# Performance work log

Measured on AMD Instinct MI355X. Metric: run time of the kernel, lower is better.

## Reference

```python
import jax, jax.numpy as jnp
import numpy as np

EMB = 1024
HEADS = 16
HEAD_DIM = EMB // HEADS
FF = 4 * EMB


def _gelu_tanh(x):
    c = jnp.sqrt(jnp.asarray(2.0 / jnp.pi, x.dtype))
    return 0.5 * x * (1.0 + jnp.tanh(c * (x + 0.044715 * x ** 3)))


def _layernorm(x, scale, shift, eps=1e-5):
    mean = jnp.mean(x, axis=-1, keepdims=True)
    var = jnp.mean((x - mean) ** 2, axis=-1, keepdims=True)
    return scale * (x - mean) / jnp.sqrt(var + eps) + shift


def setup_inputs() -> dict:
    key = jax.random.key(0)
    ks = jax.random.split(key, 8)
    s = 0.02
    return {
        "x": jax.random.normal(ks[0], (2, 2048, EMB), jnp.float32),
        "w_q": jax.random.normal(ks[1], (EMB, EMB), jnp.float32) * s,
        "w_k": jax.random.normal(ks[2], (EMB, EMB), jnp.float32) * s,
        "w_v": jax.random.normal(ks[3], (EMB, EMB), jnp.float32) * s,
        "w_o": jax.random.normal(ks[4], (EMB, EMB), jnp.float32) * s,
        "b_o": jnp.zeros((EMB,), jnp.float32),
        "ln1_scale": jnp.ones((EMB,), jnp.float32),
        "ln1_shift": jnp.zeros((EMB,), jnp.float32),
        "ln2_scale": jnp.ones((EMB,), jnp.float32),
        "ln2_shift": jnp.zeros((EMB,), jnp.float32),
        "w_ff1": jax.random.normal(ks[5], (EMB, FF), jnp.float32) * s,
        "b_ff1": jnp.zeros((FF,), jnp.float32),
        "w_ff2": jax.random.normal(ks[6], (FF, EMB), jnp.float32) * s,
        "b_ff2": jnp.zeros((EMB,), jnp.float32),
    }


def _attention(x, w_q, w_k, w_v, w_o, b_o):
    b, n, _ = x.shape
    q = (x @ w_q).reshape(b, n, HEADS, HEAD_DIM).transpose(0, 2, 1, 3)  # bhnd
    k = (x @ w_k).reshape(b, n, HEADS, HEAD_DIM).transpose(0, 2, 1, 3)
    v = (x @ w_v).reshape(b, n, HEADS, HEAD_DIM).transpose(0, 2, 1, 3)
    scores = jnp.einsum("bhqd,bhkd->bhqk", q, k)
    causal = jnp.triu(jnp.ones((n, n), bool), k=1)
    scores = jnp.where(causal, -jnp.inf, scores)
    # original scales AFTER masking (-inf stays -inf)
    attn = jax.nn.softmax(scores / jnp.sqrt(jnp.asarray(HEAD_DIM, x.dtype)), axis=-1)
    ctx = jnp.einsum("bhqk,bhkd->bhqd", attn, v)
    ctx = ctx.transpose(0, 2, 1, 3).reshape(b, n, EMB)
    return ctx @ w_o + b_o


def reference(x, w_q, w_k, w_v, w_o, b_o, ln1_scale, ln1_shift,
              ln2_scale, ln2_shift, w_ff1, b_ff1, w_ff2, b_ff2):
    h = _layernorm(x, ln1_scale, ln1_shift)
    h = _attention(h, w_q, w_k, w_v, w_o, b_o)
    x = x + h  # dropout is identity at drop_rate=0 / eval
    h = _layernorm(x, ln2_scale, ln2_shift)
    h = _gelu_tanh(h @ w_ff1 + b_ff1) @ w_ff2 + b_ff2
    return x + h
```

## Files before the change

kernel.cpp:

```cpp
#include <hip/hip_runtime.h>
#include <math.h>

#define EMB 1024
#define HEADS 16
#define HD 64
#define FF_DIM 4096
#define SEQ 2048
#define BATCH 2
#define NTOK (BATCH * SEQ)

typedef __bf16 bf16x8 __attribute__((ext_vector_type(8)));
typedef float f32x4 __attribute__((ext_vector_type(4)));

__device__ __forceinline__ unsigned short f2bf(float f) {
    union { float f; unsigned int u; } v; v.f = f;
    unsigned int r = v.u + 0x7fff + ((v.u >> 16) & 1);
    return (unsigned short)(r >> 16);
}

__device__ __forceinline__ float gelu_f(float x) {
    const float A = 1.5957691216057308f;
    const float B = 0.07135481282989427f;
    float zz = x * (A + B * x * x);
    return x * __builtin_amdgcn_rcpf(1.f + __expf(-zz));
}

#define GLOAD_LDS16(g, l)                                                      \
    __builtin_amdgcn_global_load_lds(                                          \
        (const __attribute__((address_space(1))) void*)(g),                    \
        (__attribute__((address_space(3))) void*)(l), 16, 0, 0)

__global__ __launch_bounds__(256) void ln_kernel(const float* __restrict__ x,
                                                 const float* __restrict__ scale,
                                                 const float* __restrict__ shift,
                                                 unsigned short* __restrict__ out) {
    int row = blockIdx.x;
    const float* xr = x + (size_t)row * EMB;
    unsigned short* yr = out + (size_t)row * EMB;
    int t = threadIdx.x;

    float v[4];
    float s = 0.f, s2 = 0.f;
#pragma unroll
    for (int i = 0; i < 4; i++) {
        v[i] = xr[t + i * 256];
        s += v[i];
        s2 += v[i] * v[i];
    }
    for (int o = 32; o > 0; o >>= 1) {
        s += __shfl_down(s, o, 64);
        s2 += __shfl_down(s2, o, 64);
    }
    __shared__ float red[4], red2[4];
    int wave = t >> 6;
    if ((t & 63) == 0) { red[wave] = s; red2[wave] = s2; }
    __syncthreads();
    if (t == 0) {
        float a = 0.f, b = 0.f;
#pragma unroll
        for (int i = 0; i < 4; i++) { a += red[i]; b += red2[i]; }
        red[0] = a; red2[0] = b;
    }
    __syncthreads();
    float mean = red[0] * (1.f / EMB);
    float var = red2[0] * (1.f / EMB) - mean * mean;
    float rstd = rsqrtf(var + 1e-5f);
#pragma unroll
    for (int i = 0; i < 4; i++) {
        int c = t + i * 256;
        yr[c] = f2bf(scale[c] * (v[i] - mean) * rstd + shift[c]);
    }
}

__global__ __launch_bounds__(256) void prep_kernel(
    const float* __restrict__ w0, const float* __restrict__ w1,
    const float* __restrict__ w2, const float* __restrict__ w3,
    const float* __restrict__ w4, const float* __restrict__ w5,
    unsigned short* __restrict__ o0, unsigned short* __restrict__ o1,
    unsigned short* __restrict__ o2, unsigned short* __restrict__ o3,
    unsigned short* __restrict__ o4, unsigned short* __restrict__ o5,
    const float* __restrict__ x, const float* __restrict__ ln1s,
    const float* __restrict__ ln1b, unsigned short* __restrict__ lnO) {
    __shared__ float tile[64][65];
    __shared__ float red[4], red2[4];
    int id = blockIdx.x;
    int t = threadIdx.x;

    if (id >= 3072) {
        int row = id - 3072;
        const float* xr = x + (size_t)row * EMB;
        unsigned short* yr = lnO + (size_t)row * EMB;
        float v[4];
        float s = 0.f, s2 = 0.f;
#pragma unroll
        for (int i = 0; i < 4; i++) {
            v[i] = xr[t + i * 256];
            s += v[i];
            s2 += v[i] * v[i];
        }
        for (int o = 32; o > 0; o >>= 1) {
            s += __shfl_down(s, o, 64);
            s2 += __shfl_down(s2, o, 64);
        }
        int wave = t >> 6;
        if ((t & 63) == 0) { red[wave] = s; red2[wave] = s2; }
        __syncthreads();
        if (t == 0) {
            float a = 0.f, b = 0.f;
#pragma unroll
            for (int i = 0; i < 4; i++) { a += red[i]; b += red2[i]; }
            red[0] = a; red2[0] = b;
        }
        __syncthreads();
        float mean = red[0] * (1.f / EMB);
        float var = red2[0] * (1.f / EMB) - mean * mean;
        float rstd = rsqrtf(var + 1e-5f);
#pragma unroll
        for (int i = 0; i < 4; i++) {
            int c = t + i * 256;
            yr[c] = f2bf(ln1s[c] * (v[i] - mean) * rstd + ln1b[c]);
        }
        return;
    }

    const float* src; unsigned short* dst; int K, N, lid;
    if (id < 256)       { src = w0; dst = o0; K = 1024; N = 1024; lid = id; }
    else if (id < 512)  { src = w1; dst = o1; K = 1024; N = 1024; lid = id - 256; }
    else if (id < 768)  { src = w2; dst = o2; K = 1024; N = 1024; lid = id - 512; }
    else if (id < 1024) { src = w3; dst = o3; K = 1024; N = 1024; lid = id - 768; }
    else if (id < 2048) { src = w4; dst = o4; K = 1024; N = 4096; lid = id - 1024; }
    else                { src = w5; dst = o5; K = 4096; N = 1024; lid = id - 2048; }
    int tn = N >> 6;
    int k0 = (lid / tn) << 6, n0 = (lid % tn) << 6;
    int rr = t >> 6, cc = t & 63;
#pragma unroll
    for (int i = 0; i < 16; i++) {
        int r = i * 4 + rr;
        tile[r][cc] = src[(size_t)(k0 + r) * N + n0 + cc];
    }
    __syncthreads();
#pragma unroll
    for (int i = 0; i < 16; i++) {
        int r = i * 4 + rr;
        dst[(size_t)(n0 + r) * K + k0 + cc] = f2bf(tile[cc][r]);
    }
}


__global__ __launch_bounds__(256) void ff1_gemm(
    const unsigned short* __restrict__ A,
    const unsigned short* __restrict__ Bt,
    unsigned short* __restrict__ C,
    const float* __restrict__ bias,
    int M, int N, int K) {
    __shared__ unsigned short As[2][128 * 64];
    __shared__ unsigned short Bs[2][128 * 64];

    const int t = threadIdx.x;
    const int w = t >> 6, lane = t & 63;
    const int m0 = blockIdx.x * 128, n0 = blockIdx.y * 128;

    const int srow = lane >> 3;
    const int sc = (lane & 7) ^ srow;
    const unsigned short* gA[4];
    const unsigned short* gB[4];
#pragma unroll
    for (int i = 0; i < 4; i++) {
        gA[i] = A + (size_t)(m0 + i * 32 + w * 8 + srow) * K + sc * 8;
        gB[i] = Bt + (size_t)(n0 + i * 32 + w * 8 + srow) * K + sc * 8;
    }

    const int mrow = (w >> 1) * 64, ncol = (w & 1) * 64;
    int ph[2];
#pragma unroll
    for (int s = 0; s < 2; s++) ph[s] = ((s * 4 + (lane >> 4)) ^ (lane & 7)) * 8;
    int abase[4], bbase[4];
#pragma unroll
    for (int i = 0; i < 4; i++) {
        abase[i] = (mrow + i * 16 + (lane & 15)) * 64;
        bbase[i] = (ncol + i * 16 + (lane & 15)) * 64;
    }

    f32x4 acc[4][4];
#pragma unroll
    for (int i = 0; i < 4; i++)
#pragma unroll
        for (int j = 0; j < 4; j++) acc[i][j] = (f32x4){0.f, 0.f, 0.f, 0.f};

#define STG1(b)                                                                \
    do {                                                                       \
        _Pragma("unroll") for (int i_ = 0; i_ < 4; i_++) {                     \
            GLOAD_LDS16(gA[i_], &As[b][(i_ * 32 + w * 8) * 64]);               \
            GLOAD_LDS16(gB[i_], &Bs[b][(i_ * 32 + w * 8) * 64]);               \
            gA[i_] += 64; gB[i_] += 64;                                        \
        }                                                                      \
    } while (0)

    STG1(0);
    const int nk = K >> 6;
    for (int it = 0; it < nk; it++) {
        const int buf = it & 1;
        __syncthreads();
        if (it + 1 < nk) STG1(buf ^ 1);
#pragma unroll
        for (int s = 0; s < 2; s++) {
            bf16x8 af[4], bfr[4];
#pragma unroll
            for (int i = 0; i < 4; i++) {
                af[i] = *reinterpret_cast<const bf16x8*>(&As[buf][abase[i] + ph[s]]);
                bfr[i] = *reinterpret_cast<const bf16x8*>(&Bs[buf][bbase[i] + ph[s]]);
            }
#pragma unroll
            for (int i = 0; i < 4; i++)
#pragma unroll
                for (int j = 0; j < 4; j++)
                    acc[i][j] = __builtin_amdgcn_mfma_f32_16x16x32_bf16(
                        af[i], bfr[j], acc[i][j], 0, 0, 0);
        }
    }
#undef STG1

    const int ccol = lane & 15;
    const int crow = (lane >> 4) << 2;
#pragma unroll
    for (int i = 0; i < 4; i++) {
#pragma unroll
        for (int j = 0; j < 4; j++) {
            int col = n0 + ncol + j * 16 + ccol;
            float badd = bias[col];
#pragma unroll
            for (int r = 0; r < 4; r++) {
                int row = m0 + mrow + i * 16 + crow + r;
                C[(size_t)row * N + col] = f2bf(gelu_f(acc[i][j][r] + badd));
            }
        }
    }
}

template <int EPI>
__global__ __launch_bounds__(256) void mfma_gemm_s64(
    const unsigned short* __restrict__ A,
    const unsigned short* __restrict__ Bt,
    float* __restrict__ C,
    const float* __restrict__ bias,
    const float* __restrict__ resid,
    int M, int N, int K) {
    __shared__ unsigned short As[2][64 * 64];
    __shared__ unsigned short Bs[2][64 * 64];

    const int t = threadIdx.x;
    const int w = t >> 6, lane = t & 63;
    const int m0 = blockIdx.x * 64, n0 = blockIdx.y * 64;

    const int srow = lane >> 3;
    const int sc = (lane & 7) ^ srow;
    const unsigned short* gA[2];
    const unsigned short* gB[2];
#pragma unroll
    for (int i = 0; i < 2; i++) {
        gA[i] = A + (size_t)(m0 + i * 32 + w * 8 + srow) * K + sc * 8;
        gB[i] = Bt + (size_t)(n0 + i * 32 + w * 8 + srow) * K + sc * 8;
    }

    int ph[2];
#pragma unroll
    for (int s = 0; s < 2; s++) ph[s] = ((s * 4 + (lane >> 4)) ^ (lane & 7)) * 8;
    const int mrow = (w >> 1) * 32, ncol = (w & 1) * 32;
    int abase[2], bbase[2];
#pragma unroll
    for (int i = 0; i < 2; i++) {
        abase[i] = (mrow + i * 16 + (lane & 15)) * 64;
        bbase[i] = (ncol + i * 16 + (lane & 15)) * 64;
    }

    f32x4 acc[2][2];
#pragma unroll
    for (int i = 0; i < 2; i++)
#pragma unroll
        for (int j = 0; j < 2; j++) acc[i][j] = (f32x4){0.f, 0.f, 0.f, 0.f};

#define STGS(b)                                                                \
    do {                                                                       \
        _Pragma("unroll") for (int i_ = 0; i_ < 2; i_++) {                     \
            GLOAD_LDS16(gA[i_], &As[b][(i_ * 32 + w * 8) * 64]);               \
            GLOAD_LDS16(gB[i_], &Bs[b][(i_ * 32 + w * 8) * 64]);               \
            gA[i_] += 64; gB[i_] += 64;                                        \
        }                                                                      \
    } while (0)

    STGS(0);
    const int nk = K >> 6;
    for (int it = 0; it < nk; it++) {
        const int buf = it & 1;
        __syncthreads();
        if (it + 1 < nk) STGS(buf ^ 1);
#pragma unroll
        for (int s = 0; s < 2; s++) {
            bf16x8 af[2], bfr[2];
#pragma unroll
            for (int i = 0; i < 2; i++) {
                af[i] = *reinterpret_cast<const bf16x8*>(&As[buf][abase[i] + ph[s]]);
                bfr[i] = *reinterpret_cast<const bf16x8*>(&Bs[buf][bbase[i] + ph[s]]);
            }
#pragma unroll
            for (int i = 0; i < 2; i++)
#pragma unroll
                for (int j = 0; j < 2; j++)
                    acc[i][j] = __builtin_amdgcn_mfma_f32_16x16x32_bf16(
                        af[i], bfr[j], acc[i][j], 0, 0, 0);
        }
    }
#undef STGS

    const int ccol = lane & 15;
    const int crow = (lane >> 4) << 2;
#pragma unroll
    for (int i = 0; i < 2; i++) {
#pragma unroll
        for (int j = 0; j < 2; j++) {
            int col = n0 + ncol + j * 16 + ccol;
            float badd = bias[col];
#pragma unroll
            for (int r = 0; r < 4; r++) {
                int row = m0 + mrow + i * 16 + crow + r;
                size_t idx = (size_t)row * N + col;
                if constexpr (EPI == 1) {
                    C[idx] = acc[i][j][r] + badd + resid[idx];
                } else {
                    C[idx] = C[idx] + acc[i][j][r] + badd;
                }
            }
        }
    }
}

__global__ __launch_bounds__(256) void qkv_gemm(
    const unsigned short* __restrict__ lnO,
    const unsigned short* __restrict__ wqkT,
    const unsigned short* __restrict__ wvT,
    unsigned short* __restrict__ q,
    unsigned short* __restrict__ kb,
    unsigned short* __restrict__ vT) {
    __shared__ unsigned short As[2][128 * 64];
    __shared__ unsigned short Bs[2][128 * 64];

    const int t = threadIdx.x;
    const int w = t >> 6, lane = t & 63;
    const int bid = blockIdx.x;
    const bool qk = bid < 512;

    const unsigned short *A, *Bt;
    int m0, n0, N;
    if (qk) {
        A = lnO; Bt = wqkT;
        m0 = (bid & 31) * 128; n0 = (bid >> 5) * 128; N = 2048;
    } else {
        int lb = bid - 512;
        A = wvT; Bt = lnO;
        m0 = (lb & 7) * 128; n0 = (lb >> 3) * 128; N = 4096;
    }
    const int K = 1024;

    const int srow = lane >> 3;
    const int sc = (lane & 7) ^ srow;
    const unsigned short* gA[4];
    const unsigned short* gB[4];
#pragma unroll
    for (int i = 0; i < 4; i++) {
        gA[i] = A + (size_t)(m0 + i * 32 + w * 8 + srow) * K + sc * 8;
        gB[i] = Bt + (size_t)(n0 + i * 32 + w * 8 + srow) * K + sc * 8;
    }

    const int mrow = (w >> 1) * 64, ncol = (w & 1) * 64;
    int ph[2];
#pragma unroll
    for (int s = 0; s < 2; s++) ph[s] = ((s * 4 + (lane >> 4)) ^ (lane & 7)) * 8;
    int abase[4], bbase[4];
#pragma unroll
    for (int i = 0; i < 4; i++) {
        abase[i] = (mrow + i * 16 + (lane & 15)) * 64;
        bbase[i] = (ncol + i * 16 + (lane & 15)) * 64;
    }

    f32x4 acc[4][4];
#pragma unroll
    for (int i = 0; i < 4; i++)
#pragma unroll
        for (int j = 0; j < 4; j++) acc[i][j] = (f32x4){0.f, 0.f, 0.f, 0.f};

#define STGQ(b)                                                                \
    do {                                                                       \
        _Pragma("unroll") for (int i_ = 0; i_ < 4; i_++) {                     \
            GLOAD_LDS16(gA[i_], &As[b][(i_ * 32 + w * 8) * 64]);               \
            GLOAD_LDS16(gB[i_], &Bs[b][(i_ * 32 + w * 8) * 64]);               \
            gA[i_] += 64; gB[i_] += 64;                                        \
        }                                                                      \
    } while (0)

    STGQ(0);
    const int nk = K >> 6;
    for (int it = 0; it < nk; it++) {
        const int buf = it & 1;
        __syncthreads();
        if (it + 1 < nk) STGQ(buf ^ 1);
#pragma unroll
        for (int s = 0; s < 2; s++) {
            bf16x8 af[4], bfr[4];
#pragma unroll
            for (int i = 0; i < 4; i++) {
                af[i] = *reinterpret_cast<const bf16x8*>(&As[buf][abase[i] + ph[s]]);
                bfr[i] = *reinterpret_cast<const bf16x8*>(&Bs[buf][bbase[i] + ph[s]]);
            }
#pragma unroll
            for (int i = 0; i < 4; i++)
#pragma unroll
                for (int j = 0; j < 4; j++)
                    acc[i][j] = __builtin_amdgcn_mfma_f32_16x16x32_bf16(
                        af[i], bfr[j], acc[i][j], 0, 0, 0);
        }
    }
#undef STGQ

    const int ccol = lane & 15;
    const int crow = (lane >> 4) << 2;
    unsigned short* dst;
    int nbase;
    if (qk) {
        dst = (n0 < 1024) ? q : kb;
        nbase = n0 & 1023;
    } else {
        dst = vT;
        nbase = n0;
    }
    const int ldc = qk ? 1024 : 4096;
#pragma unroll
    for (int i = 0; i < 4; i++) {
#pragma unroll
        for (int j = 0; j < 4; j++) {
            int col = nbase + ncol + j * 16 + ccol;
#pragma unroll
            for (int r = 0; r < 4; r++) {
                int row = m0 + mrow + i * 16 + crow + r;
                dst[(size_t)row * ldc + col] = f2bf(acc[i][j][r]);
            }
        }
    }
}

__global__ __launch_bounds__(256) void attn_mfma(
    const unsigned short* __restrict__ Q,
    const unsigned short* __restrict__ K,
    const unsigned short* __restrict__ Vt,
    unsigned short* __restrict__ O) {
    __shared__ unsigned short Ks[2][64 * 64];
    __shared__ unsigned short Vs[2][64 * 64];
    __shared__ unsigned short Ps[4][16 * 64];

    const int t = threadIdx.x;
    const int w = t >> 6, lane = t & 63;
    const int l15 = lane & 15, l4 = lane >> 4;
    const int bh = blockIdx.x;
    const int b = bh >> 4, h = bh & 15;
    const int pair = blockIdx.y;

    const int sr = (w << 3) + (lane >> 3);
    const int sc = lane & 7;
    const int c = sc ^ (sr & 7);
    const unsigned short* kbase = K + ((size_t)(b * SEQ)) * EMB + h * HD;
    const unsigned short* vbase = Vt + ((size_t)(h * HD)) * (size_t)NTOK + (size_t)b * SEQ;
    unsigned short* Pw = &Ps[w][0];

#define STAGE(k0s, buf)                                                        \
    do {                                                                       \
        GLOAD_LDS16(kbase + (size_t)((k0s) + sr) * EMB + c * 8,                \
                    &Ks[buf][(w << 3) * 64]);                                  \
        GLOAD_LDS16(kbase + (size_t)((k0s) + sr + 32) * EMB + c * 8,           \
                    &Ks[buf][((w << 3) + 32) * 64]);                           \
        GLOAD_LDS16(vbase + (size_t)sr * NTOK + (k0s) + c * 8,                 \
                    &Vs[buf][(w << 3) * 64]);                                  \
        GLOAD_LDS16(vbase + (size_t)(sr + 32) * NTOK + (k0s) + c * 8,          \
                    &Vs[buf][((w << 3) + 32) * 64]);                           \
    } while (0)

    const float C1 = 0.125f * 1.4426950408889634f;
    const float C2 = 3.0f * 1.4426950408889634f;

#pragma unroll
    for (int phase = 0; phase < 2; phase++) {
        const int qt = phase ? pair : (31 - pair);
        const int q0 = qt * 64;

        const unsigned short* qg =
            Q + ((size_t)(b * SEQ + q0 + w * 16 + l15)) * EMB + h * HD + l4 * 8;
        bf16x8 qf0 = *(const bf16x8*)qg;
        bf16x8 qf1 = *(const bf16x8*)(qg + 32);
        const int qrow_c = q0 + w * 16 + l4 * 4;

        float lsum[4] = {0.f, 0.f, 0.f, 0.f};
        f32x4 Oacc[4];
#pragma unroll
        for (int j = 0; j < 4; j++) Oacc[j] = (f32x4){0.f, 0.f, 0.f, 0.f};

        const int ntiles = qt + 1;
        __syncthreads();
        STAGE(0, 0);
        for (int tile = 0; tile < ntiles; tile++) {
            const int k0 = tile * 64;
            const int buf = tile & 1;
            __syncthreads();
            if (tile + 1 < ntiles) STAGE(k0 + 64, buf ^ 1);

            f32x4 S[4];
#pragma unroll
            for (int j = 0; j < 4; j++) S[j] = (f32x4){0.f, 0.f, 0.f, 0.f};
#pragma unroll
            for (int s = 0; s < 2; s++) {
                bf16x8 qf = s ? qf1 : qf0;
#pragma unroll
                for (int j = 0; j < 4; j++) {
                    int rk = 16 * j + l15;
                    int phys = (s * 4 + l4) ^ (rk & 7);
                    bf16x8 kf = *(const bf16x8*)&Ks[buf][rk * 64 + phys * 8];
                    S[j] = __builtin_amdgcn_mfma_f32_16x16x32_bf16(qf, kf, S[j], 0, 0, 0);
                }
            }

            if (tile == ntiles - 1) {
#pragma unroll
                for (int j = 0; j < 4; j++)
#pragma unroll
                    for (int r = 0; r < 4; r++) {
                        float e = exp2f(S[j][r] * C1 - C2);
                        if (k0 + 16 * j + l15 > qrow_c + r) e = 0.f;
                        S[j][r] = e;
                        lsum[r] += e;
                    }
            } else {
#pragma unroll
                for (int j = 0; j < 4; j++)
#pragma unroll
                    for (int r = 0; r < 4; r++) {
                        float e = exp2f(S[j][r] * C1 - C2);
                        S[j][r] = e;
                        lsum[r] += e;
                    }
            }

#pragma unroll
            for (int r = 0; r < 4; r++) {
                int row = l4 * 4 + r;
#pragma unroll
                for (int j = 0; j < 4; j++) {
                    int col = 16 * j + l15;
                    int phys = (col >> 3) ^ (row & 7);
                    Pw[row * 64 + phys * 8 + (col & 7)] = f2bf(S[j][r]);
                }
            }

#pragma unroll
            for (int s = 0; s < 2; s++) {
                int pphys = (s * 4 + l4) ^ (l15 & 7);
                bf16x8 pf = *(const bf16x8*)&Pw[l15 * 64 + pphys * 8];
#pragma unroll
                for (int j = 0; j < 4; j++) {
                    int rv = 16 * j + l15;
                    int vphys = (s * 4 + l4) ^ (rv & 7);
                    bf16x8 vf = *(const bf16x8*)&Vs[buf][rv * 64 + vphys * 8];
                    Oacc[j] = __builtin_amdgcn_mfma_f32_16x16x32_bf16(pf, vf, Oacc[j], 0, 0, 0);
                }
            }
        }

#pragma unroll
        for (int r = 0; r < 4; r++) {
            float l = lsum[r];
#pragma unroll
            for (int off = 1; off < 16; off <<= 1)
                l += __shfl_xor(l, off, 64);
            float inv = 1.f / l;
            size_t rowb = (size_t)(b * SEQ + qrow_c + r) * EMB + h * HD;
#pragma unroll
            for (int j = 0; j < 4; j++)
                O[rowb + 16 * j + l15] = f2bf(Oacc[j][r] * inv);
        }
    }
#undef STAGE
}

extern "C" void kernel_launch(void* const* d_in, const int* in_sizes, int n_in,
                              void* d_out, int out_size, void* d_ws, size_t ws_size,
                              hipStream_t stream) {
    const float* x     = (const float*)d_in[0];
    const float* w_q   = (const float*)d_in[1];
    const float* w_k   = (const float*)d_in[2];
    const float* w_v   = (const float*)d_in[3];
    const float* w_o   = (const float*)d_in[4];
    const float* b_o   = (const float*)d_in[5];
    const float* ln1s  = (const float*)d_in[6];
    const float* ln1b  = (const float*)d_in[7];
    const float* ln2s  = (const float*)d_in[8];
    const float* ln2b  = (const float*)d_in[9];
    const float* w_ff1 = (const float*)d_in[10];
    const float* b_ff1 = (const float*)d_in[11];
    const float* w_ff2 = (const float*)d_in[12];
    const float* b_ff2 = (const float*)d_in[13];
    float* out = (float*)d_out;

    char* p = (char*)d_ws;
    unsigned short* lnO  = (unsigned short*)p; p += (size_t)NTOK * EMB * 2;
    unsigned short* q    = (unsigned short*)p; p += (size_t)NTOK * EMB * 2;
    unsigned short* kbuf = (unsigned short*)p; p += (size_t)NTOK * EMB * 2;
    unsigned short* vT   = (unsigned short*)p; p += (size_t)NTOK * EMB * 2;
    unsigned short* ctx  = (unsigned short*)p; p += (size_t)NTOK * EMB * 2;
    unsigned short* ff1a = (unsigned short*)p; p += (size_t)NTOK * FF_DIM * 2;
    unsigned short* wqkT = (unsigned short*)p; p += (size_t)2 * EMB * EMB * 2;
    unsigned short* wvT  = (unsigned short*)p; p += (size_t)EMB * EMB * 2;
    unsigned short* woT  = (unsigned short*)p; p += (size_t)EMB * EMB * 2;
    unsigned short* wf1T = (unsigned short*)p; p += (size_t)FF_DIM * EMB * 2;
    unsigned short* wf2T = (unsigned short*)p; p += (size_t)EMB * FF_DIM * 2;

    dim3 blk(256);
    dim3 gS64(NTOK / 64, EMB / 64);
    dim3 gFF1(NTOK / 128, FF_DIM / 128);
    dim3 gAttn(BATCH * HEADS, 16);

    prep_kernel<<<3072 + NTOK, blk, 0, stream>>>(
        w_q, w_k, w_v, w_o, w_ff1, w_ff2,
        wqkT, wqkT + (size_t)EMB * EMB, wvT, woT, wf1T, wf2T,
        x, ln1s, ln1b, lnO);
    qkv_gemm<<<768, blk, 0, stream>>>(lnO, wqkT, wvT, q, kbuf, vT);
    attn_mfma<<<gAttn, blk, 0, stream>>>(q, kbuf, vT, ctx);
    mfma_gemm_s64<1><<<gS64, blk, 0, stream>>>(ctx, woT, out, b_o, x, NTOK, EMB, EMB);
    ln_kernel<<<NTOK, blk, 0, stream>>>(out, ln2s, ln2b, ctx);
    ff1_gemm<<<gFF1, blk, 0, stream>>>(ctx, wf1T, ff1a, b_ff1, NTOK, FF_DIM, EMB);
    mfma_gemm_s64<3><<<gS64, blk, 0, stream>>>(ff1a, wf2T, out, b_ff2, nullptr, NTOK, EMB, FF_DIM);
}
```

Before: 331.0 us.

## Add 128x128 FF2 GEMM kernel and transpose attention MFMA layout for packed stores

Replaces the 64x64-tiled FF2 GEMM (K=4096) with a dedicated 128x128-tile kernel using double-buffered global-to-LDS loads. This raises operand reuse per block and reduces the block count to 256. In attention, the MFMA operands are swapped so each lane holds four consecutive key columns. That lets P be written to LDS and O to global memory with packed bf16 conversions and 8-byte stores, and it replaces the per-row 16-lane shuffle reductions with two shuffles. The risk is that 256 blocks may underfill the GPU's compute units, and the larger accumulator tile raises register pressure.

```diff
diff --git a/kernel.cpp b/kernel.cpp
--- a/kernel.cpp
+++ b/kernel.cpp
@@ -16,6 +16,12 @@
     union { float f; unsigned int u; } v; v.f = f;
     unsigned int r = v.u + 0x7fff + ((v.u >> 16) & 1);
     return (unsigned short)(r >> 16);
+}
+
+__device__ __forceinline__ unsigned int cvt_pk_bf16(float a, float b) {
+    unsigned int r;
+    asm("v_cvt_pk_bf16_f32 %0, %1, %2" : "=v"(r) : "v"(a), "v"(b));
+    return r;
 }
 
 __device__ __forceinline__ float gelu_f(float x) {
@@ -237,6 +243,98 @@
     }
 }
 
+__global__ __launch_bounds__(256) void ff2_gemm(
+    const unsigned short* __restrict__ A,
+    const unsigned short* __restrict__ Bt,
+    float* __restrict__ C,
+    const float* __restrict__ bias,
+    int M, int N, int K) {
+    __shared__ unsigned short As[2][128 * 64];
+    __shared__ unsigned short Bs[2][128 * 64];
+
+    const int t = threadIdx.x;
+    const int w = t >> 6, lane = t & 63;
+    const int id = blockIdx.x;
+    const int m0 = (id >> 3) * 128, n0 = (id & 7) * 128;
+
+    const int srow = lane >> 3;
+    const int sc = (lane & 7) ^ srow;
+    const unsigned short* gA[4];
+    const unsigned short* gB[4];
+#pragma unroll
+    for (int i = 0; i < 4; i++) {
+        gA[i] = A + (size_t)(m0 + i * 32 + w * 8 + srow) * K + sc * 8;
+        gB[i] = Bt + (size_t)(n0 + i * 32 + w * 8 + srow) * K + sc * 8;
+    }
+
+    const int mrow = (w >> 1) * 64, ncol = (w & 1) * 64;
+    int ph[2];
+#pragma unroll
+    for (int s = 0; s < 2; s++) ph[s] = ((s * 4 + (lane >> 4)) ^ (lane & 7)) * 8;
+    int abase[4], bbase[4];
+#pragma unroll
+    for (int i = 0; i < 4; i++) {
+        abase[i] = (mrow + i * 16 + (lane & 15)) * 64;
+        bbase[i] = (ncol + i * 16 + (lane & 15)) * 64;
+    }
+
+    f32x4 acc[4][4];
+#pragma unroll
+    for (int i = 0; i < 4; i++)
+#pragma unroll
+        for (int j = 0; j < 4; j++) acc[i][j] = (f32x4){0.f, 0.f, 0.f, 0.f};
+
+#define STG2(b)                                                                \
+    do {                                                                       \
+        _Pragma("unroll") for (int i_ = 0; i_ < 4; i_++) {                     \
+            GLOAD_LDS16(gA[i_], &As[b][(i_ * 32 + w * 8) * 64]);               \
+            GLOAD_LDS16(gB[i_], &Bs[b][(i_ * 32 + w * 8) * 64]);               \
+            gA[i_] += 64; gB[i_] += 64;                                        \
+        }                                                                      \
+    } while (0)
+
+    STG2(0);
+    const int nk = K >> 6;
+    for (int it = 0; it < nk; it++) {
+        const int buf = it & 1;
+        __syncthreads();
+        if (it + 1 < nk) STG2(buf ^ 1);
+#pragma unroll
+        for (int s = 0; s < 2; s++) {
+            bf16x8 af[4], bfr[4];
+#pragma unroll
+            for (int i = 0; i < 4; i++) {
+                af[i] = *reinterpret_cast<const bf16x8*>(&As[buf][abase[i] + ph[s]]);
+                bfr[i] = *reinterpret_cast<const bf16x8*>(&Bs[buf][bbase[i] + ph[s]]);
+            }
+#pragma unroll
+            for (int i = 0; i < 4; i++)
+#pragma unroll
+                for (int j = 0; j < 4; j++)
+                    acc[i][j] = __builtin_amdgcn_mfma_f32_16x16x32_bf16(
+                        af[i], bfr[j], acc[i][j], 0, 0, 0);
+        }
+    }
+#undef STG2
+
+    const int ccol = lane & 15;
+    const int crow = (lane >> 4) << 2;
+#pragma unroll
+    for (int i = 0; i < 4; i++) {
+#pragma unroll
+        for (int j = 0; j < 4; j++) {
+            int col = n0 + ncol + j * 16 + ccol;
+            float badd = bias[col];
+#pragma unroll
+            for (int r = 0; r < 4; r++) {
+                int row = m0 + mrow + i * 16 + crow + r;
+                size_t idx = (size_t)row * N + col;
+                C[idx] = C[idx] + acc[i][j][r] + badd;
+            }
+        }
+    }
+}
+
 template <int EPI>
 __global__ __launch_bounds__(256) void mfma_gemm_s64(
     const unsigned short* __restrict__ A,
@@ -494,9 +592,9 @@
             Q + ((size_t)(b * SEQ + q0 + w * 16 + l15)) * EMB + h * HD + l4 * 8;
         bf16x8 qf0 = *(const bf16x8*)qg;
         bf16x8 qf1 = *(const bf16x8*)(qg + 32);
-        const int qrow_c = q0 + w * 16 + l4 * 4;
-
-        float lsum[4] = {0.f, 0.f, 0.f, 0.f};
+        const int qrow = q0 + w * 16 + l15;
+
+        float ls[4] = {0.f, 0.f, 0.f, 0.f};
         f32x4 Oacc[4];
 #pragma unroll
         for (int j = 0; j < 4; j++) Oacc[j] = (f32x4){0.f, 0.f, 0.f, 0.f};
@@ -521,7 +619,7 @@
                     int rk = 16 * j + l15;
                     int phys = (s * 4 + l4) ^ (rk & 7);
                     bf16x8 kf = *(const bf16x8*)&Ks[buf][rk * 64 + phys * 8];
-                    S[j] = __builtin_amdgcn_mfma_f32_16x16x32_bf16(qf, kf, S[j], 0, 0, 0);
+                    S[j] = __builtin_amdgcn_mfma_f32_16x16x32_bf16(kf, qf, S[j], 0, 0, 0);
                 }
             }
 
@@ -531,57 +629,52 @@
 #pragma unroll
                     for (int r = 0; r < 4; r++) {
                         float e = exp2f(S[j][r] * C1 - C2);
-                        if (k0 + 16 * j + l15 > qrow_c + r) e = 0.f;
+                        if (k0 + 16 * j + 4 * l4 + r > qrow) e = 0.f;
                         S[j][r] = e;
-                        lsum[r] += e;
                     }
             } else {
 #pragma unroll
                 for (int j = 0; j < 4; j++)
 #pragma unroll
-                    for (int r = 0; r < 4; r++) {
-                        float e = exp2f(S[j][r] * C1 - C2);
-                        S[j][r] = e;
-                        lsum[r] += e;
-                    }
-            }
-
-#pragma unroll
-            for (int r = 0; r < 4; r++) {
-                int row = l4 * 4 + r;
-#pragma unroll
-                for (int j = 0; j < 4; j++) {
-                    int col = 16 * j + l15;
-                    int phys = (col >> 3) ^ (row & 7);
-                    Pw[row * 64 + phys * 8 + (col & 7)] = f2bf(S[j][r]);
-                }
+                    for (int r = 0; r < 4; r++)
+                        S[j][r] = exp2f(S[j][r] * C1 - C2);
+            }
+
+#pragma unroll
+            for (int j = 0; j < 4; j++) {
+                ls[j] += S[j][0] + S[j][1] + S[j][2] + S[j][3];
+                unsigned int lo = cvt_pk_bf16(S[j][0], S[j][1]);
+                unsigned int hi = cvt_pk_bf16(S[j][2], S[j][3]);
+                int chunk = (2 * j + (l4 >> 1)) ^ (l15 & 7);
+                uint2 val; val.x = lo; val.y = hi;
+                *reinterpret_cast<uint2*>(&Pw[l15 * 64 + chunk * 8 + (l4 & 1) * 4]) = val;
             }
 
 #pragma unroll
             for (int s = 0; s < 2; s++) {
-                int pphys = (s * 4 + l4) ^ (l15 & 7);
-                bf16x8 pf = *(const bf16x8*)&Pw[l15 * 64 + pphys * 8];
+                int pch = (4 * s + l4) ^ (l15 & 7);
+                bf16x8 pf = *(const bf16x8*)&Pw[l15 * 64 + pch * 8];
 #pragma unroll
                 for (int j = 0; j < 4; j++) {
                     int rv = 16 * j + l15;
-                    int vphys = (s * 4 + l4) ^ (rv & 7);
-                    bf16x8 vf = *(const bf16x8*)&Vs[buf][rv * 64 + vphys * 8];
-                    Oacc[j] = __builtin_amdgcn_mfma_f32_16x16x32_bf16(pf, vf, Oacc[j], 0, 0, 0);
+                    int vph = (s * 4 + l4) ^ (rv & 7);
+                    bf16x8 vf = *(const bf16x8*)&Vs[buf][rv * 64 + vph * 8];
+                    Oacc[j] = __builtin_amdgcn_mfma_f32_16x16x32_bf16(vf, pf, Oacc[j], 0, 0, 0);
                 }
             }
         }
 
-#pragma unroll
-        for (int r = 0; r < 4; r++) {
-            float l = lsum[r];
-#pragma unroll
-            for (int off = 1; off < 16; off <<= 1)
-                l += __shfl_xor(l, off, 64);
-            float inv = 1.f / l;
-            size_t rowb = (size_t)(b * SEQ + qrow_c + r) * EMB + h * HD;
-#pragma unroll
-            for (int j = 0; j < 4; j++)
-                O[rowb + 16 * j + l15] = f2bf(Oacc[j][r] * inv);
+        float l = ls[0] + ls[1] + ls[2] + ls[3];
+        l += __shfl_xor(l, 16, 64);
+        l += __shfl_xor(l, 32, 64);
+        float inv = 1.f / l;
+        size_t rowb = (size_t)(b * SEQ + qrow) * EMB + h * HD;
+#pragma unroll
+        for (int j = 0; j < 4; j++) {
+            unsigned int lo = cvt_pk_bf16(Oacc[j][0] * inv, Oacc[j][1] * inv);
+            unsigned int hi = cvt_pk_bf16(Oacc[j][2] * inv, Oacc[j][3] * inv);
+            uint2 val; val.x = lo; val.y = hi;
+            *reinterpret_cast<uint2*>(&O[rowb + 16 * j + 4 * l4]) = val;
         }
     }
 #undef STAGE
@@ -633,5 +726,5 @@
     mfma_gemm_s64<1><<<gS64, blk, 0, stream>>>(ctx, woT, out, b_o, x, NTOK, EMB, EMB);
     ln_kernel<<<NTOK, blk, 0, stream>>>(out, ln2s, ln2b, ctx);
     ff1_gemm<<<gFF1, blk, 0, stream>>>(ctx, wf1T, ff1a, b_ff1, NTOK, FF_DIM, EMB);
-    mfma_gemm_s64<3><<<gS64, blk, 0, stream>>>(ff1a, wf2T, out, b_ff2, nullptr, NTOK, EMB, FF_DIM);
-}
+    ff2_gemm<<<256, blk, 0, stream>>>(ff1a, wf2T, out, b_ff2, NTOK, EMB, FF_DIM);
+}
```

Result: slower. 354.1 us (+7.0%).

## Transpose attention MFMA operands for packed P writes and vectorize layernorm

Applied to the files above, without the earlier changes.

Swaps the A/B operands of both attention MFMAs so each lane holds four consecutive key columns of one query row. P can then be written to LDS as packed bf16 pairs (v_cvt_pk_bf16) in 8-byte stores instead of scalar stores, and the output is written with vector stores. The row-sum reduction needs only two shuffles, and s_setprio is raised around the MFMA blocks. The layernorm kernels switch to float4 loads and ushort4 stores. This targets LDS store count and softmax overhead in the attention inner loop. It relies on the inline-asm conversion rounding the same way as the software f2bf.

```diff
diff --git a/kernel.cpp b/kernel.cpp
--- a/kernel.cpp
+++ b/kernel.cpp
@@ -18,6 +18,12 @@
     return (unsigned short)(r >> 16);
 }
 
+__device__ __forceinline__ unsigned int cvt_pk_bf16(float a, float b) {
+    unsigned int r;
+    asm("v_cvt_pk_bf16_f32 %0, %1, %2" : "=v"(r) : "v"(a), "v"(b));
+    return r;
+}
+
 __device__ __forceinline__ float gelu_f(float x) {
     const float A = 1.5957691216057308f;
     const float B = 0.07135481282989427f;
@@ -35,18 +41,12 @@
                                                  const float* __restrict__ shift,
                                                  unsigned short* __restrict__ out) {
     int row = blockIdx.x;
-    const float* xr = x + (size_t)row * EMB;
-    unsigned short* yr = out + (size_t)row * EMB;
+    const float4* xr = (const float4*)(x + (size_t)row * EMB);
     int t = threadIdx.x;
 
-    float v[4];
-    float s = 0.f, s2 = 0.f;
-#pragma unroll
-    for (int i = 0; i < 4; i++) {
-        v[i] = xr[t + i * 256];
-        s += v[i];
-        s2 += v[i] * v[i];
-    }
+    float4 v = xr[t];
+    float s = v.x + v.y + v.z + v.w;
+    float s2 = v.x * v.x + v.y * v.y + v.z * v.z + v.w * v.w;
     for (int o = 32; o > 0; o >>= 1) {
         s += __shfl_down(s, o, 64);
         s2 += __shfl_down(s2, o, 64);
@@ -65,11 +65,15 @@
     float mean = red[0] * (1.f / EMB);
     float var = red2[0] * (1.f / EMB) - mean * mean;
     float rstd = rsqrtf(var + 1e-5f);
-#pragma unroll
-    for (int i = 0; i < 4; i++) {
-        int c = t + i * 256;
-        yr[c] = f2bf(scale[c] * (v[i] - mean) * rstd + shift[c]);
-    }
+
+    float4 sc = ((const float4*)scale)[t];
+    float4 sh = ((const float4*)shift)[t];
+    ushort4 o;
+    o.x = f2bf(sc.x * (v.x - mean) * rstd + sh.x);
+    o.y = f2bf(sc.y * (v.y - mean) * rstd + sh.y);
+    o.z = f2bf(sc.z * (v.z - mean) * rstd + sh.z);
+    o.w = f2bf(sc.w * (v.w - mean) * rstd + sh.w);
+    ((ushort4*)(out + (size_t)row * EMB))[t] = o;
 }
 
 __global__ __launch_bounds__(256) void prep_kernel(
@@ -88,16 +92,10 @@
 
     if (id >= 3072) {
         int row = id - 3072;
-        const float* xr = x + (size_t)row * EMB;
-        unsigned short* yr = lnO + (size_t)row * EMB;
-        float v[4];
-        float s = 0.f, s2 = 0.f;
-#pragma unroll
-        for (int i = 0; i < 4; i++) {
-            v[i] = xr[t + i * 256];
-            s += v[i];
-            s2 += v[i] * v[i];
-        }
+        const float4* xr = (const float4*)(x + (size_t)row * EMB);
+        float4 v = xr[t];
+        float s = v.x + v.y + v.z + v.w;
+        float s2 = v.x * v.x + v.y * v.y + v.z * v.z + v.w * v.w;
         for (int o = 32; o > 0; o >>= 1) {
             s += __shfl_down(s, o, 64);
             s2 += __shfl_down(s2, o, 64);
@@ -115,11 +113,15 @@
         float mean = red[0] * (1.f / EMB);
         float var = red2[0] * (1.f / EMB) - mean * mean;
         float rstd = rsqrtf(var + 1e-5f);
-#pragma unroll
-        for (int i = 0; i < 4; i++) {
-            int c = t + i * 256;
-            yr[c] = f2bf(ln1s[c] * (v[i] - mean) * rstd + ln1b[c]);
-        }
+
+        float4 sc = ((const float4*)ln1s)[t];
+        float4 sh = ((const float4*)ln1b)[t];
+        ushort4 o;
+        o.x = f2bf(sc.x * (v.x - mean) * rstd + sh.x);
+        o.y = f2bf(sc.y * (v.y - mean) * rstd + sh.y);
+        o.z = f2bf(sc.z * (v.z - mean) * rstd + sh.z);
+        o.w = f2bf(sc.w * (v.w - mean) * rstd + sh.w);
+        ((ushort4*)(lnO + (size_t)row * EMB))[t] = o;
         return;
     }
 
@@ -494,9 +496,9 @@
             Q + ((size_t)(b * SEQ + q0 + w * 16 + l15)) * EMB + h * HD + l4 * 8;
         bf16x8 qf0 = *(const bf16x8*)qg;
         bf16x8 qf1 = *(const bf16x8*)(qg + 32);
-        const int qrow_c = q0 + w * 16 + l4 * 4;
-
-        float lsum[4] = {0.f, 0.f, 0.f, 0.f};
+        const int qrow = q0 + w * 16 + l15;
+
+        float ls[4] = {0.f, 0.f, 0.f, 0.f};
         f32x4 Oacc[4];
 #pragma unroll
         for (int j = 0; j < 4; j++) Oacc[j] = (f32x4){0.f, 0.f, 0.f, 0.f};
@@ -513,6 +515,7 @@
             f32x4 S[4];
 #pragma unroll
             for (int j = 0; j < 4; j++) S[j] = (f32x4){0.f, 0.f, 0.f, 0.f};
+            __builtin_amdgcn_s_setprio(1);
 #pragma unroll
             for (int s = 0; s < 2; s++) {
                 bf16x8 qf = s ? qf1 : qf0;
@@ -521,9 +524,10 @@
                     int rk = 16 * j + l15;
                     int phys = (s * 4 + l4) ^ (rk & 7);
                     bf16x8 kf = *(const bf16x8*)&Ks[buf][rk * 64 + phys * 8];
-                    S[j] = __builtin_amdgcn_mfma_f32_16x16x32_bf16(qf, kf, S[j], 0, 0, 0);
+                    S[j] = __builtin_amdgcn_mfma_f32_16x16x32_bf16(kf, qf, S[j], 0, 0, 0);
                 }
             }
+            __builtin_amdgcn_s_setprio(0);
 
             if (tile == ntiles - 1) {
 #pragma unroll
@@ -531,57 +535,54 @@
 #pragma unroll
                     for (int r = 0; r < 4; r++) {
                         float e = exp2f(S[j][r] * C1 - C2);
-                        if (k0 + 16 * j + l15 > qrow_c + r) e = 0.f;
+                        if (k0 + 16 * j + 4 * l4 + r > qrow) e = 0.f;
                         S[j][r] = e;
-                        lsum[r] += e;
                     }
             } else {
 #pragma unroll
                 for (int j = 0; j < 4; j++)
 #pragma unroll
-                    for (int r = 0; r < 4; r++) {
-                        float e = exp2f(S[j][r] * C1 - C2);
-                        S[j][r] = e;
-                        lsum[r] += e;
-                    }
-            }
-
-#pragma unroll
-            for (int r = 0; r < 4; r++) {
-                int row = l4 * 4 + r;
-#pragma unroll
-                for (int j = 0; j < 4; j++) {
-                    int col = 16 * j + l15;
-                    int phys = (col >> 3) ^ (row & 7);
-                    Pw[row * 64 + phys * 8 + (col & 7)] = f2bf(S[j][r]);
-                }
-            }
-
+                    for (int r = 0; r < 4; r++)
+                        S[j][r] = exp2f(S[j][r] * C1 - C2);
+            }
+
+#pragma unroll
+            for (int j = 0; j < 4; j++) {
+                ls[j] += S[j][0] + S[j][1] + S[j][2] + S[j][3];
+                unsigned int lo = cvt_pk_bf16(S[j][0], S[j][1]);
+                unsigned int hi = cvt_pk_bf16(S[j][2], S[j][3]);
+                int chunk = (2 * j + (l4 >> 1)) ^ (l15 & 7);
+                uint2 val; val.x = lo; val.y = hi;
+                *reinterpret_cast<uint2*>(&Pw[l15 * 64 + chunk * 8 + (l4 & 1) * 4]) = val;
+            }
+
+            __builtin_amdgcn_s_setprio(1);
 #pragma unroll
             for (int s = 0; s < 2; s++) {
-                int pphys = (s * 4 + l4) ^ (l15 & 7);
-                bf16x8 pf = *(const bf16x8*)&Pw[l15 * 64 + pphys * 8];
+                int pch = (4 * s + l4) ^ (l15 & 7);
+                bf16x8 pf = *(const bf16x8*)&Pw[l15 * 64 + pch * 8];
 #pragma unroll
                 for (int j = 0; j < 4; j++) {
                     int rv = 16 * j + l15;
-                    int vphys = (s * 4 + l4) ^ (rv & 7);
-                    bf16x8 vf = *(const bf16x8*)&Vs[buf][rv * 64 + vphys * 8];
-                    Oacc[j] = __builtin_amdgcn_mfma_f32_16x16x32_bf16(pf, vf, Oacc[j], 0, 0, 0);
+                    int vph = (s * 4 + l4) ^ (rv & 7);
+                    bf16x8 vf = *(const bf16x8*)&Vs[buf][rv * 64 + vph * 8];
+                    Oacc[j] = __builtin_amdgcn_mfma_f32_16x16x32_bf16(vf, pf, Oacc[j], 0, 0, 0);
                 }
             }
-        }
-
-#pragma unroll
-        for (int r = 0; r < 4; r++) {
-            float l = lsum[r];
-#pragma unroll
-            for (int off = 1; off < 16; off <<= 1)
-                l += __shfl_xor(l, off, 64);
-            float inv = 1.f / l;
-            size_t rowb = (size_t)(b * SEQ + qrow_c + r) * EMB + h * HD;
-#pragma unroll
-            for (int j = 0; j < 4; j++)
-                O[rowb + 16 * j + l15] = f2bf(Oacc[j][r] * inv);
+            __builtin_amdgcn_s_setprio(0);
+        }
+
+        float l = ls[0] + ls[1] + ls[2] + ls[3];
+        l += __shfl_xor(l, 16, 64);
+        l += __shfl_xor(l, 32, 64);
+        float inv = 1.f / l;
+        size_t rowb = (size_t)(b * SEQ + qrow) * EMB + h * HD;
+#pragma unroll
+        for (int j = 0; j < 4; j++) {
+            unsigned int lo = cvt_pk_bf16(Oacc[j][0] * inv, Oacc[j][1] * inv);
+            unsigned int hi = cvt_pk_bf16(Oacc[j][2] * inv, Oacc[j][3] * inv);
+            uint2 val; val.x = lo; val.y = hi;
+            *reinterpret_cast<uint2*>(&O[rowb + 16 * j + 4 * l4]) = val;
         }
     }
 #undef STAGE
```

New measurement: 327.3 us. About the same (-1.1%).
